# Kernel optimization log

Measured on AMD Instinct MI355X. Metric: run time of the kernel, lower is better.

The kernel has to match this reference:

```python
import jax, jax.numpy as jnp
import numpy as np

B, C, H, W = 32, 3072, 28, 28   # concatenated layer4(upsampled)+layer3 features of ResNet-50 @448px
K = 11                          # num_cpt concepts (prototypes)
NC = 200                        # num_classes (CUB-200)


def setup_inputs() -> dict:
    key = jax.random.key(0)
    k0, k1, k2 = jax.random.split(key, 3)
    x = jax.random.normal(k0, (B, C, H, W), dtype=jnp.float32)
    # fc_landmarks: 1x1 conv, no bias -> weight (K, C)
    w_land = jax.random.normal(k1, (K, C), dtype=jnp.float32) * 0.02
    # modulation parameter, initialized to ones in the module
    modulation = jnp.ones((1, C, K), dtype=jnp.float32)
    # fc_class_landmarks: Linear(C -> NC), no bias -> weight (NC, C)
    w_cls = jax.random.normal(k2, (NC, C), dtype=jnp.float32) * 0.02
    return {"x": x, "w_land": w_land, "modulation": modulation, "w_cls": w_cls}


def reference(x, w_land, modulation, w_cls):
    # ab = fc_landmarks(x): 1x1 conv == channel contraction
    ab = jnp.einsum('bchw,kc->bkhw', x, w_land)                      # (B,K,H,W)
    b_sq = jnp.sum(x * x, axis=1, keepdims=True)                     # (B,1,H,W)
    a_sq = jnp.sum(w_land * w_land, axis=1)[None, :, None, None]     # (1,K,1,1)
    # squared distance ||x - w||^2 = b_sq - 2ab + a_sq; softmax over concepts of -dist
    maps = jax.nn.softmax(-(b_sq - 2.0 * ab + a_sq), axis=1)         # (B,K,H,W)
    attn_cls = jnp.sum(maps, axis=(-2, -1))                          # (B,K)
    # (maps.unsqueeze(1) * x.unsqueeze(2)).mean(-1).mean(-1) == batched contraction over HW
    hw = maps.shape[-2] * maps.shape[-1]
    all_features = jnp.einsum('bkhw,bchw->bck', maps, x) / hw        # (B,C,K)
    all_features_modulated = all_features * modulation               # (B,C,K)
    # eval mode: Dropout1d is identity
    scores = jnp.einsum('bck,nc->bnk', all_features_modulated, w_cls)  # (B,NC,K)
    scores = jnp.sum(scores, axis=-1)                                # (B,NC)
    return all_features_modulated, scores, maps, attn_cls
```

## Files before the change

kernel.cpp:

```cpp
#include <hip/hip_runtime.h>

constexpr int B  = 32;
constexpr int C  = 3072;
constexpr int HW = 784;
constexpr int K  = 11;
constexpr int NC = 200;

constexpr int AFM_OFF    = 0;
constexpr int SCORES_OFF = 1081344;
constexpr int MAPS_OFF   = 1087744;
constexpr int ATTN_OFF   = 1363712;

constexpr int WT_OFF   = 0;
constexpr int ASQ_OFF  = 36864;
constexpr int FSUM_OFF = 36880;

__global__ __launch_bounds__(256) void k0_prep(const float* __restrict__ w_land,
                                               float* __restrict__ ws,
                                               float* __restrict__ attn) {
  const int bid = blockIdx.x;
  const int t = threadIdx.x;
  if (bid < K) {
    const int k = bid;
    float s = 0.f;
    for (int c = t; c < C; c += 256) {
      float v = w_land[k * C + c];
      s = fmaf(v, v, s);
    }
    __shared__ float red[256];
    red[t] = s;
    __syncthreads();
    for (int off = 128; off > 0; off >>= 1) {
      if (t < off) red[t] += red[t + off];
      __syncthreads();
    }
    if (t == 0) ws[ASQ_OFF + k] = red[0];
  } else if (bid < K + C / 256) {
    const int c = (bid - K) * 256 + t;
    #pragma unroll
    for (int k = 0; k < K; k++)
      ws[WT_OFF + c * 12 + k] = 2.f * w_land[k * C + c];
    ws[WT_OFF + c * 12 + K] = 0.f;
  } else {
    for (int i = t; i < B * K; i += 256) attn[i] = 0.f;
  }
}

__global__ __launch_bounds__(512) void k1_maps(const float* __restrict__ x,
                                               const float* __restrict__ ws,
                                               float* __restrict__ maps_out,
                                               float* __restrict__ attn_out) {
  const int bid  = blockIdx.x;
  const int b    = bid / 13;
  const int tile = bid % 13;
  const int t    = threadIdx.x;
  const int g    = __builtin_amdgcn_readfirstlane(t >> 6);
  const int hwl  = t & 63;
  const int hw   = tile * 64 + hwl;
  const int hwc  = hw < HW ? hw : HW - 1;

  const float* xp  = x + (size_t)b * C * HW + hwc;
  const float* wT  = ws + WT_OFF;
  const float* asq = ws + ASQ_OFF;

  float acc[K];
  #pragma unroll
  for (int k = 0; k < K; k++) acc[k] = (g == 0) ? -asq[k] : 0.f;

  for (int i0 = 0; i0 < C / 8; i0 += 16) {
    float xv[16];
    #pragma unroll
    for (int u = 0; u < 16; u++)
      xv[u] = xp[(size_t)((i0 + u) * 8 + g) * HW];
    #pragma unroll
    for (int u = 0; u < 16; u++) {
      const float* wrow = wT + ((i0 + u) * 8 + g) * 12;
      #pragma unroll
      for (int k = 0; k < K; k++) acc[k] = fmaf(wrow[k], xv[u], acc[k]);
    }
  }

  __shared__ float abp[8][K][64];
  #pragma unroll
  for (int k = 0; k < K; k++) abp[g][k][hwl] = acc[k];
  __syncthreads();

  if (g == 0) {
    float l[K];
    #pragma unroll
    for (int k = 0; k < K; k++) {
      float s = 0.f;
      #pragma unroll
      for (int gg = 0; gg < 8; gg++) s += abp[gg][k][hwl];
      l[k] = s;
    }
    float m = l[0];
    #pragma unroll
    for (int k = 1; k < K; k++) m = fmaxf(m, l[k]);
    float z = 0.f;
    #pragma unroll
    for (int k = 0; k < K; k++) { l[k] = __expf(l[k] - m); z += l[k]; }
    const float inv = 1.f / z;
    const bool valid = hw < HW;
    #pragma unroll
    for (int k = 0; k < K; k++) {
      float r = l[k] * inv;
      if (valid) maps_out[((size_t)b * K + k) * HW + hw] = r;
      float v = valid ? r : 0.f;
      #pragma unroll
      for (int sh = 32; sh > 0; sh >>= 1) v += __shfl_xor(v, sh);
      if (hwl == 0) atomicAdd(&attn_out[b * K + k], v);
    }
  }
}

constexpr int CT   = 128;
constexpr int XROW = 68;
constexpr int MROW = 832;

__global__ __launch_bounds__(256) void k2_feat(const float* __restrict__ x,
                                               const float* __restrict__ maps_g,
                                               const float* __restrict__ modulation,
                                               float* __restrict__ afm_out,
                                               float* __restrict__ fsum) {
  __shared__ __align__(16) float maps_s[K * MROW];
  __shared__ __align__(16) float lds_x[CT * XROW];

  const int bid = blockIdx.x;
  const int b   = (B - 1) - (bid / (C / CT));
  const int c0  = (bid % (C / CT)) * CT;
  const int t   = threadIdx.x;

  for (int k = 0; k < K; k++)
    for (int i = t; i < MROW; i += 256)
      maps_s[k * MROW + i] = (i < HW) ? maps_g[((size_t)b * K + k) * HW + i] : 0.f;

  const int hwl = t & 63;
  const int rr  = t >> 6;
  const int p   = t & 63;
  const int q   = t >> 6;

  float f0[K], f1[K];
  #pragma unroll
  for (int k = 0; k < K; k++) { f0[k] = 0.f; f1[k] = 0.f; }

  const float* xb = x + (size_t)b * C * HW;

  for (int ch = 0; ch < 13; ch++) {
    const int hbase = ch * 64;
    __syncthreads();
    #pragma unroll
    for (int i = 0; i < CT / 4; i++) {
      const int r = rr + i * 4;
      int hwp = hbase + hwl;
      if (hwp >= HW) hwp = HW - 1;
      lds_x[r * XROW + hwl] = xb[(size_t)(c0 + r) * HW + hwp];
    }
    __syncthreads();
    #pragma unroll
    for (int hg = 0; hg < 4; hg++) {
      const int hoff = (q * 4 + hg) * 4;
      const float4 xa = *(const float4*)&lds_x[p * XROW + hoff];
      const float4 xc = *(const float4*)&lds_x[(p + 64) * XROW + hoff];
      #pragma unroll
      for (int k = 0; k < K; k++) {
        const float4 m4 = *(const float4*)&maps_s[k * MROW + hbase + hoff];
        f0[k] += xa.x * m4.x + xa.y * m4.y + xa.z * m4.z + xa.w * m4.w;
        f1[k] += xc.x * m4.x + xc.y * m4.y + xc.z * m4.z + xc.w * m4.w;
      }
    }
  }

  __syncthreads();
  float* fbuf = lds_x;
  float* fred = maps_s;
  #pragma unroll
  for (int k = 0; k < K; k++) {
    fbuf[(q * CT + p) * K + k]      = f0[k];
    fbuf[(q * CT + p + 64) * K + k] = f1[k];
  }
  __syncthreads();

  const float inv_hw = 1.f / (float)HW;
  for (int o = t; o < CT * K; o += 256) {
    float s = fbuf[o] + fbuf[CT * K + o] + fbuf[2 * CT * K + o] + fbuf[3 * CT * K + o];
    s = s * inv_hw * modulation[c0 * K + o];
    fred[o] = s;
    afm_out[(size_t)b * C * K + c0 * K + o] = s;
  }
  __syncthreads();
  if (t < CT) {
    float s = 0.f;
    #pragma unroll
    for (int k = 0; k < K; k++) s += fred[t * K + k];
    fsum[(size_t)b * C + c0 + t] = s;
  }
}

__global__ __launch_bounds__(256) void k4_scores(const float* __restrict__ fsum,
                                                 const float* __restrict__ w_cls,
                                                 float* __restrict__ scores) {
  __shared__ float fs[C];
  const int bid = blockIdx.x;
  const int b   = bid / (NC / 8);
  const int nt  = bid % (NC / 8);
  const int t   = threadIdx.x;

  for (int i = t; i < C; i += 256) fs[i] = fsum[b * C + i];
  __syncthreads();

  const int nl = t >> 5, lane = t & 31;
  const int n = nt * 8 + nl;
  const float* wr = w_cls + (size_t)n * C;
  float acc = 0.f;
  for (int c = lane; c < C; c += 32) acc = fmaf(wr[c], fs[c], acc);
  #pragma unroll
  for (int sh = 16; sh > 0; sh >>= 1) acc += __shfl_xor(acc, sh);
  if (lane == 0) scores[b * NC + n] = acc;
}

extern "C" void kernel_launch(void* const* d_in, const int* in_sizes, int n_in,
                              void* d_out, int out_size, void* d_ws, size_t ws_size,
                              hipStream_t stream) {
  const float* x          = (const float*)d_in[0];
  const float* w_land     = (const float*)d_in[1];
  const float* modulation = (const float*)d_in[2];
  const float* w_cls      = (const float*)d_in[3];

  float* out    = (float*)d_out;
  float* afm    = out + AFM_OFF;
  float* scores = out + SCORES_OFF;
  float* maps   = out + MAPS_OFF;
  float* attn   = out + ATTN_OFF;
  float* ws     = (float*)d_ws;

  k0_prep  <<<K + C / 256 + 1, 256, 0, stream>>>(w_land, ws, attn);
  k1_maps  <<<B * 13,          512, 0, stream>>>(x, ws, maps, attn);
  k2_feat  <<<B * (C / CT),    256, 0, stream>>>(x, maps, modulation, afm, ws + FSUM_OFF);
  k4_scores<<<B * (NC / 8),    256, 0, stream>>>(ws + FSUM_OFF, w_cls, scores);
}
```

Measured before the change: 562.5 us.

## Split landmark projection into channel-chunk partials and retile feature pooling

The distance projection kernel now has each block cover a 192-channel chunk across all 784 spatial positions and write partial sums to workspace. A separate small kernel reduces the partials and computes the softmax, maps and attention sums. The feature-pooling kernel is retiled to 384 channels per block, staging full spatial rows in dynamic LDS and reducing with wave shuffles, so x rows are read in contiguous coalesced spans. This adds an extra launch and a partial-sum round trip through global memory, and cuts the pooling grid to 256 blocks, which may hurt occupancy.

```diff
diff --git a/kernel.cpp b/kernel.cpp
--- a/kernel.cpp
+++ b/kernel.cpp
@@ -14,6 +14,8 @@
 constexpr int WT_OFF   = 0;
 constexpr int ASQ_OFF  = 36864;
 constexpr int FSUM_OFF = 36880;
+constexpr int PART_OFF = 135184;
+constexpr int PSTRIDE  = K * HW;
 
 __global__ __launch_bounds__(256) void k0_prep(const float* __restrict__ w_land,
                                                float* __restrict__ ws,
@@ -46,154 +48,185 @@
   }
 }
 
-__global__ __launch_bounds__(512) void k1_maps(const float* __restrict__ x,
+__global__ __launch_bounds__(512) void k1a_part(const float* __restrict__ x,
+                                                const float* __restrict__ ws,
+                                                float* __restrict__ part) {
+  const int bid = blockIdx.x;
+  const int b   = bid >> 4;
+  const int cc  = bid & 15;
+  const int c0  = cc * 192;
+  const int t   = threadIdx.x;
+  const bool pred = t < (HW - 512);
+
+  const float* xs = x + ((size_t)b * C + c0) * HW;
+  const float* wp = ws + WT_OFF + c0 * 12;
+
+  float a0[K], a1[K];
+  #pragma unroll
+  for (int k = 0; k < K; k++) { a0[k] = 0.f; a1[k] = 0.f; }
+
+  #pragma unroll 2
+  for (int c = 0; c < 192; c++) {
+    float v0 = xs[(size_t)c * HW + t];
+    float v1 = pred ? xs[(size_t)c * HW + 512 + t] : 0.f;
+    #pragma unroll
+    for (int k = 0; k < K; k++) {
+      float wv = wp[c * 12 + k];
+      a0[k] = fmaf(wv, v0, a0[k]);
+      a1[k] = fmaf(wv, v1, a1[k]);
+    }
+  }
+
+  float* pp = part + (size_t)(b * 16 + cc) * PSTRIDE;
+  #pragma unroll
+  for (int k = 0; k < K; k++) {
+    pp[k * HW + t] = a0[k];
+    if (pred) pp[k * HW + 512 + t] = a1[k];
+  }
+}
+
+__global__ __launch_bounds__(64) void k1b_soft(const float* __restrict__ part,
                                                const float* __restrict__ ws,
                                                float* __restrict__ maps_out,
                                                float* __restrict__ attn_out) {
   const int bid  = blockIdx.x;
   const int b    = bid / 13;
   const int tile = bid % 13;
-  const int t    = threadIdx.x;
-  const int g    = __builtin_amdgcn_readfirstlane(t >> 6);
-  const int hwl  = t & 63;
-  const int hw   = tile * 64 + hwl;
-  const int hwc  = hw < HW ? hw : HW - 1;
-
-  const float* xp  = x + (size_t)b * C * HW + hwc;
-  const float* wT  = ws + WT_OFF;
+  const int lane = threadIdx.x;
+  const int hw   = tile * 64 + lane;
+  const bool valid = hw < HW;
+
   const float* asq = ws + ASQ_OFF;
-
-  float acc[K];
-  #pragma unroll
-  for (int k = 0; k < K; k++) acc[k] = (g == 0) ? -asq[k] : 0.f;
-
-  for (int i0 = 0; i0 < C / 8; i0 += 16) {
-    float xv[16];
-    #pragma unroll
-    for (int u = 0; u < 16; u++)
-      xv[u] = xp[(size_t)((i0 + u) * 8 + g) * HW];
-    #pragma unroll
-    for (int u = 0; u < 16; u++) {
-      const float* wrow = wT + ((i0 + u) * 8 + g) * 12;
-      #pragma unroll
-      for (int k = 0; k < K; k++) acc[k] = fmaf(wrow[k], xv[u], acc[k]);
-    }
-  }
-
-  __shared__ float abp[8][K][64];
-  #pragma unroll
-  for (int k = 0; k < K; k++) abp[g][k][hwl] = acc[k];
-  __syncthreads();
-
-  if (g == 0) {
-    float l[K];
-    #pragma unroll
-    for (int k = 0; k < K; k++) {
-      float s = 0.f;
-      #pragma unroll
-      for (int gg = 0; gg < 8; gg++) s += abp[gg][k][hwl];
-      l[k] = s;
-    }
-    float m = l[0];
-    #pragma unroll
-    for (int k = 1; k < K; k++) m = fmaxf(m, l[k]);
-    float z = 0.f;
-    #pragma unroll
-    for (int k = 0; k < K; k++) { l[k] = __expf(l[k] - m); z += l[k]; }
-    const float inv = 1.f / z;
-    const bool valid = hw < HW;
-    #pragma unroll
-    for (int k = 0; k < K; k++) {
-      float r = l[k] * inv;
-      if (valid) maps_out[((size_t)b * K + k) * HW + hw] = r;
-      float v = valid ? r : 0.f;
-      #pragma unroll
-      for (int sh = 32; sh > 0; sh >>= 1) v += __shfl_xor(v, sh);
-      if (hwl == 0) atomicAdd(&attn_out[b * K + k], v);
-    }
-  }
-}
-
-constexpr int CT   = 128;
-constexpr int XROW = 68;
-constexpr int MROW = 832;
-
-__global__ __launch_bounds__(256) void k2_feat(const float* __restrict__ x,
+  const float* pb  = part + (size_t)b * 16 * PSTRIDE;
+
+  float l[K];
+  #pragma unroll
+  for (int k = 0; k < K; k++) l[k] = -asq[k];
+  for (int cc = 0; cc < 16; cc++) {
+    #pragma unroll
+    for (int k = 0; k < K; k++)
+      l[k] += pb[cc * PSTRIDE + k * HW + hw];
+  }
+
+  float m = l[0];
+  #pragma unroll
+  for (int k = 1; k < K; k++) m = fmaxf(m, l[k]);
+  float z = 0.f;
+  #pragma unroll
+  for (int k = 0; k < K; k++) { l[k] = __expf(l[k] - m); z += l[k]; }
+  const float inv = 1.f / z;
+  #pragma unroll
+  for (int k = 0; k < K; k++) {
+    float r = l[k] * inv;
+    if (valid) maps_out[((size_t)b * K + k) * HW + hw] = r;
+    float v = valid ? r : 0.f;
+    #pragma unroll
+    for (int sh = 32; sh > 0; sh >>= 1) v += __shfl_xor(v, sh);
+    if (lane == 0) atomicAdd(&attn_out[b * K + k], v);
+  }
+}
+
+constexpr int XST = 836;
+constexpr int MST = 788;
+constexpr int XC_FLOATS = 16 * XST;
+constexpr int MS_FLOATS = K * MST;
+constexpr int FS_FLOATS = 384 * K;
+constexpr int K2_LDS_BYTES = (XC_FLOATS + MS_FLOATS + FS_FLOATS) * 4;
+
+__global__ __launch_bounds__(512) void k2_feat(const float* __restrict__ x,
                                                const float* __restrict__ maps_g,
                                                const float* __restrict__ modulation,
                                                float* __restrict__ afm_out,
                                                float* __restrict__ fsum) {
-  __shared__ __align__(16) float maps_s[K * MROW];
-  __shared__ __align__(16) float lds_x[CT * XROW];
-
-  const int bid = blockIdx.x;
-  const int b   = (B - 1) - (bid / (C / CT));
-  const int c0  = (bid % (C / CT)) * CT;
+  extern __shared__ float smem[];
+  float* xc     = smem;
+  float* maps_s = smem + XC_FLOATS;
+  float* f_s    = smem + XC_FLOATS + MS_FLOATS;
+
+  const int bid = blockIdx.x;
+  const int b   = (B - 1) - (bid >> 3);
+  const int c0  = (bid & 7) * 384;
   const int t   = threadIdx.x;
+  const int w   = t >> 6;
+  const int lane = t & 63;
 
   for (int k = 0; k < K; k++)
-    for (int i = t; i < MROW; i += 256)
-      maps_s[k * MROW + i] = (i < HW) ? maps_g[((size_t)b * K + k) * HW + i] : 0.f;
-
-  const int hwl = t & 63;
-  const int rr  = t >> 6;
-  const int p   = t & 63;
-  const int q   = t >> 6;
-
-  float f0[K], f1[K];
-  #pragma unroll
-  for (int k = 0; k < K; k++) { f0[k] = 0.f; f1[k] = 0.f; }
-
-  const float* xb = x + (size_t)b * C * HW;
-
-  for (int ch = 0; ch < 13; ch++) {
-    const int hbase = ch * 64;
+    for (int i = t; i < HW; i += 512)
+      maps_s[k * MST + i] = maps_g[((size_t)b * K + k) * HW + i];
+
+  const float* xb = x + ((size_t)b * C + c0) * HW;
+  const int cA = 2 * w, cB = 2 * w + 1;
+  const bool pred = t < (HW - 512);
+
+  for (int ch = 0; ch < 24; ch++) {
     __syncthreads();
-    #pragma unroll
-    for (int i = 0; i < CT / 4; i++) {
-      const int r = rr + i * 4;
-      int hwp = hbase + hwl;
-      if (hwp >= HW) hwp = HW - 1;
-      lds_x[r * XROW + hwl] = xb[(size_t)(c0 + r) * HW + hwp];
+    const float* xrow = xb + (size_t)ch * 16 * HW;
+    #pragma unroll
+    for (int r = 0; r < 16; r++) {
+      float v0 = xrow[(size_t)r * HW + t];
+      xc[r * XST + t] = v0;
+      if (pred) xc[r * XST + 512 + t] = xrow[(size_t)r * HW + 512 + t];
     }
     __syncthreads();
-    #pragma unroll
-    for (int hg = 0; hg < 4; hg++) {
-      const int hoff = (q * 4 + hg) * 4;
-      const float4 xa = *(const float4*)&lds_x[p * XROW + hoff];
-      const float4 xc = *(const float4*)&lds_x[(p + 64) * XROW + hoff];
+
+    float a0[K], a1[K];
+    #pragma unroll
+    for (int k = 0; k < K; k++) { a0[k] = 0.f; a1[k] = 0.f; }
+
+    const float* xr0 = xc + cA * XST;
+    const float* xr1 = xc + cB * XST;
+    #pragma unroll
+    for (int g = 0; g < 3; g++) {
+      const int off = g * 256 + lane * 4;
+      const float4 x0 = *(const float4*)(xr0 + off);
+      const float4 x1 = *(const float4*)(xr1 + off);
       #pragma unroll
       for (int k = 0; k < K; k++) {
-        const float4 m4 = *(const float4*)&maps_s[k * MROW + hbase + hoff];
-        f0[k] += xa.x * m4.x + xa.y * m4.y + xa.z * m4.z + xa.w * m4.w;
-        f1[k] += xc.x * m4.x + xc.y * m4.y + xc.z * m4.z + xc.w * m4.w;
-      }
-    }
-  }
-
+        const float4 m4 = *(const float4*)(maps_s + k * MST + off);
+        a0[k] += x0.x * m4.x + x0.y * m4.y + x0.z * m4.z + x0.w * m4.w;
+        a1[k] += x1.x * m4.x + x1.y * m4.y + x1.z * m4.z + x1.w * m4.w;
+      }
+    }
+    if (lane < 16) {
+      const int off = 768 + lane;
+      const float x0 = xr0[off], x1 = xr1[off];
+      #pragma unroll
+      for (int k = 0; k < K; k++) {
+        const float ms = maps_s[k * MST + off];
+        a0[k] = fmaf(x0, ms, a0[k]);
+        a1[k] = fmaf(x1, ms, a1[k]);
+      }
+    }
+
+    #pragma unroll
+    for (int k = 0; k < K; k++) {
+      #pragma unroll
+      for (int sh = 32; sh > 0; sh >>= 1) {
+        a0[k] += __shfl_xor(a0[k], sh);
+        a1[k] += __shfl_xor(a1[k], sh);
+      }
+    }
+    if (lane == 0) {
+      #pragma unroll
+      for (int k = 0; k < K; k++) {
+        f_s[(ch * 16 + cA) * K + k] = a0[k];
+        f_s[(ch * 16 + cB) * K + k] = a1[k];
+      }
+    }
+  }
   __syncthreads();
-  float* fbuf = lds_x;
-  float* fred = maps_s;
-  #pragma unroll
-  for (int k = 0; k < K; k++) {
-    fbuf[(q * CT + p) * K + k]      = f0[k];
-    fbuf[(q * CT + p + 64) * K + k] = f1[k];
-  }
-  __syncthreads();
 
   const float inv_hw = 1.f / (float)HW;
-  for (int o = t; o < CT * K; o += 256) {
-    float s = fbuf[o] + fbuf[CT * K + o] + fbuf[2 * CT * K + o] + fbuf[3 * CT * K + o];
-    s = s * inv_hw * modulation[c0 * K + o];
-    fred[o] = s;
+  for (int o = t; o < 384 * K; o += 512) {
+    float s = f_s[o] * inv_hw * modulation[c0 * K + o];
     afm_out[(size_t)b * C * K + c0 * K + o] = s;
   }
-  __syncthreads();
-  if (t < CT) {
+  if (t < 384) {
     float s = 0.f;
     #pragma unroll
-    for (int k = 0; k < K; k++) s += fred[t * K + k];
-    fsum[(size_t)b * C + c0 + t] = s;
+    for (int k = 0; k < K; k++)
+      s += f_s[t * K + k] * modulation[(c0 + t) * K + k];
+    fsum[(size_t)b * C + c0 + t] = s * inv_hw;
   }
 }
 
@@ -233,9 +266,18 @@
   float* maps   = out + MAPS_OFF;
   float* attn   = out + ATTN_OFF;
   float* ws     = (float*)d_ws;
+  float* part   = ws + PART_OFF;
+
+  static bool attr_set = false;
+  if (!attr_set) {
+    hipFuncSetAttribute((const void*)k2_feat,
+                        hipFuncAttributeMaxDynamicSharedMemorySize, K2_LDS_BYTES);
+    attr_set = true;
+  }
 
   k0_prep  <<<K + C / 256 + 1, 256, 0, stream>>>(w_land, ws, attn);
-  k1_maps  <<<B * 13,          512, 0, stream>>>(x, ws, maps, attn);
-  k2_feat  <<<B * (C / CT),    256, 0, stream>>>(x, maps, modulation, afm, ws + FSUM_OFF);
+  k1a_part <<<B * 16,          512, 0, stream>>>(x, ws, part);
+  k1b_soft <<<B * 13,          64,  0, stream>>>(part, ws, maps, attn);
+  k2_feat  <<<B * 8,           512, K2_LDS_BYTES, stream>>>(x, maps, modulation, afm, ws + FSUM_OFF);
   k4_scores<<<B * (NC / 8),    256, 0, stream>>>(ws + FSUM_OFF, w_cls, scores);
 }
```

New measurement: 803.1 us. 1.43x slower.
